# Optimization experiments

Measured on AMD Instinct MI355X. Metric: run time of the kernel, lower is better.

Reference implementation:

```python
import jax, jax.numpy as jnp
import numpy as np

MAX_DEPTH = 12  # 2^12-1 = 4095 internal nodes, 4096 leaves
NUM_INPUT = 1024
NUM_OUTPUT = 1024
BATCH = 4096


def setup_inputs() -> dict:
    key = jax.random.key(0)
    k1, k2, k3 = jax.random.split(key, 3)
    n_internal = (1 << MAX_DEPTH) - 1
    n_leaves = 1 << MAX_DEPTH
    x = jax.random.normal(k1, (BATCH, NUM_INPUT), dtype=jnp.float32)
    # per-node weights ~ N(0, 0.1) as in nn.Parameter(torch.empty(num_input).normal_(0, 0.1))
    W = jax.random.normal(k2, (n_internal, NUM_INPUT), dtype=jnp.float32) * 0.1
    b = jnp.zeros((n_internal,), dtype=jnp.float32)
    # leaf prob_dist initialized to ones in the original
    leaf = jnp.ones((n_leaves, NUM_OUTPUT), dtype=jnp.float32)
    # use random leaves so the blend is non-trivial for correctness checking
    leaf = leaf + jax.random.normal(k3, (n_leaves, NUM_OUTPUT), dtype=jnp.float32)
    return {"x": x, "W": W, "b": b, "leaf": leaf}


def reference(x, W, b, leaf):
    # W rows are internal nodes in level order: [root | level1 (2) | level2 (4) | ...]
    # Gate value at each node: sigmoid(x . w + b); output blends right with weight g,
    # left with weight (1-g), recursively -> leaf mixture weights are products of
    # gate / (1-gate) along each root-to-leaf path.
    B = x.shape[0]
    g = jax.nn.sigmoid(jnp.einsum('bi,ni->bn', x, W) + b)  # [B, n_internal]
    probs = jnp.ones((B, 1), dtype=x.dtype)
    idx = 0
    for d in range(MAX_DEPTH):  # structural loop over tree levels (fixed, small)
        n = 1 << d
        gl = g[:, idx:idx + n]  # gates at level d, [B, n]
        idx += n
        # children interleaved: [L0, R0, L1, R1, ...]; left weight (1-g), right g
        probs = jnp.stack([probs * (1.0 - gl), probs * gl], axis=-1).reshape(B, 2 * n)
    # output = sum over leaves of path_prob * leaf_dist
    out = jnp.einsum('bl,lo->bo', probs, leaf)  # [B, num_output]
    return out
```

## Files before the change

kernel.cpp:

```cpp
#include <hip/hip_runtime.h>
#include <hip/hip_bf16.h>
#include <hip/hip_fp16.h>

typedef _Float16 half8 __attribute__((ext_vector_type(8)));
typedef _Float16 half4 __attribute__((ext_vector_type(4)));
typedef float floatx4 __attribute__((ext_vector_type(4)));

#define BATCH   4096
#define NIN     1024
#define NODES   4095
#define NPAD    4096
#define NOUT    1024
#define NLEAF   4096
#define SPLITK  4

__device__ __forceinline__ void gload_lds16(const void* g, void* l) {
    __builtin_amdgcn_global_load_lds(
        (const __attribute__((address_space(1))) void*)g,
        (__attribute__((address_space(3))) void*)l, 16, 0, 0);
}

__global__ void k_f32_to_f16_pad(const float* __restrict__ src,
                                 _Float16* __restrict__ dst, int n, int nsrc) {
    int i = (blockIdx.x * blockDim.x + threadIdx.x) * 4;
    if (i >= n) return;
    float4 v;
    if (i < nsrc) v = *(const float4*)(src + i);
    else          v = make_float4(0.f, 0.f, 0.f, 0.f);
    half4 h;
    h.x = (_Float16)v.x; h.y = (_Float16)v.y;
    h.z = (_Float16)v.z; h.w = (_Float16)v.w;
    *(half4*)(dst + i) = h;
}

__global__ void k_transpose_f16(const float* __restrict__ src,
                                _Float16* __restrict__ dst) {
    __shared__ _Float16 t[32][33];
    int l0 = blockIdx.x * 32, o0 = blockIdx.y * 32;
    int tx = threadIdx.x & 31, ty = threadIdx.x >> 5;
#pragma unroll
    for (int i = 0; i < 4; i++) {
        int l = l0 + ty + i * 8;
        t[ty + i * 8][tx] = (_Float16)src[(size_t)l * NOUT + o0 + tx];
    }
    __syncthreads();
#pragma unroll
    for (int i = 0; i < 4; i++) {
        int o = o0 + ty + i * 8;
        dst[(size_t)o * NLEAF + l0 + tx] = t[tx][ty + i * 8];
    }
}

template <int EPILOGUE>
__launch_bounds__(1024, 4)
__global__ void gemm256(const _Float16* __restrict__ A,
                        const _Float16* __restrict__ Bm,
                        const float* __restrict__ bias,
                        void* __restrict__ C,
                        int M, int N, int K, int ldc, int Klen) {
    __shared__ __align__(16) _Float16 As[2][2][2][4096];
    __shared__ __align__(16) _Float16 Bs[2][2][2][4096];
    const int tid  = threadIdx.x;
    const int lane = tid & 63;
    const int wid  = tid >> 6;
    const int wm   = wid >> 2;
    const int wn   = wid & 3;
    const int m0 = blockIdx.y * 256;
    const int n0 = blockIdx.x * 256;
    const int k0 = blockIdx.z * Klen;
    (void)N;

    floatx4 acc[4][4] = {};

    const int hh = tid >> 9;
    const int rr = (tid >> 2) & 127;
    const int pp = tid & 3;
    const int cc = pp ^ ((tid >> 3) & 3);
    const _Float16* Abase = A  + (size_t)(m0 + hh * 128 + rr) * K + k0 + cc * 8;
    const _Float16* Bbase = Bm + (size_t)(n0 + hh * 128 + rr) * K + k0 + cc * 8;
    const int dsl = (tid & 511) * 8;

    auto stageA = [&](int bufx, int s, int T) {
        gload_lds16(Abase + T * 64 + s * 32, &As[bufx][hh][s][dsl]);
    };
    auto stageB = [&](int bufx, int s, int T) {
        gload_lds16(Bbase + T * 64 + s * 32, &Bs[bufx][hh][s][dsl]);
    };

    const int l15 = lane & 15;
    const int l4  = lane >> 4;
    const int pos = (l4 ^ ((l15 >> 1) & 3)) * 8;
    const int ra  = (wm & 1) * 64 + l15;
    const int rb  = (wn & 1) * 64 + l15;
    const int ah  = wm >> 1;
    const int bh  = wn >> 1;

    const int NTt = Klen >> 6;

    stageA(0, 0, 0); stageA(0, 1, 0); stageB(0, 0, 0); stageB(0, 1, 0);
    __syncthreads();

    int buf = 0;
    for (int T = 0; T < NTt; ++T) {
        if (T + 1 < NTt) {
            stageA(buf ^ 1, 0, T + 1); stageA(buf ^ 1, 1, T + 1);
            stageB(buf ^ 1, 0, T + 1); stageB(buf ^ 1, 1, T + 1);
        }
#pragma unroll
        for (int s = 0; s < 2; s++) {
            const _Float16* Ab = &As[buf][ah][s][0];
            const _Float16* Bb = &Bs[buf][bh][s][0];
            half8 af[4], bf[4];
#pragma unroll
            for (int fi = 0; fi < 4; fi++)
                af[fi] = *(const half8*)(Ab + (ra + fi * 16) * 32 + pos);
#pragma unroll
            for (int fj = 0; fj < 4; fj++)
                bf[fj] = *(const half8*)(Bb + (rb + fj * 16) * 32 + pos);
#pragma unroll
            for (int fi = 0; fi < 4; fi++)
#pragma unroll
                for (int fj = 0; fj < 4; fj++)
                    acc[fi][fj] = __builtin_amdgcn_mfma_f32_16x16x32_f16(
                        af[fi], bf[fj], acc[fi][fj], 0, 0, 0);
        }
        __syncthreads();
        buf ^= 1;
    }

    _Float16* Cp = (_Float16*)C + (EPILOGUE == 2 ? (size_t)blockIdx.z * M * ldc : 0);
#pragma unroll
    for (int fi = 0; fi < 4; fi++)
#pragma unroll
        for (int fj = 0; fj < 4; fj++) {
            const int col = n0 + wn * 64 + fj * 16 + l15;
            float bb = 0.f;
            if (EPILOGUE == 1) bb = (col < NODES) ? bias[col] : 0.f;
#pragma unroll
            for (int rj = 0; rj < 4; rj++) {
                const int row = m0 + wm * 64 + fi * 16 + l4 * 4 + rj;
                float v = acc[fi][fj][rj];
                if (EPILOGUE == 1) {
                    float z = v + bb;
                    Cp[(size_t)row * ldc + col] = (_Float16)(1.f / (1.f + __expf(-z)));
                } else {
                    Cp[(size_t)row * ldc + col] = (_Float16)v;
                }
            }
        }
}

__global__ void k_reduce4(const _Float16* __restrict__ part, float* __restrict__ out) {
    const size_t S = (size_t)BATCH * NOUT;
    size_t i = ((size_t)blockIdx.x * 256 + threadIdx.x) * 8;
    half8 a = *(const half8*)(part + i);
    half8 b = *(const half8*)(part + S + i);
    half8 c = *(const half8*)(part + 2 * S + i);
    half8 d = *(const half8*)(part + 3 * S + i);
    float4 lo, hi;
    lo.x = (float)a[0] + (float)b[0] + (float)c[0] + (float)d[0];
    lo.y = (float)a[1] + (float)b[1] + (float)c[1] + (float)d[1];
    lo.z = (float)a[2] + (float)b[2] + (float)c[2] + (float)d[2];
    lo.w = (float)a[3] + (float)b[3] + (float)c[3] + (float)d[3];
    hi.x = (float)a[4] + (float)b[4] + (float)c[4] + (float)d[4];
    hi.y = (float)a[5] + (float)b[5] + (float)c[5] + (float)d[5];
    hi.z = (float)a[6] + (float)b[6] + (float)c[6] + (float)d[6];
    hi.w = (float)a[7] + (float)b[7] + (float)c[7] + (float)d[7];
    *(float4*)(out + i) = lo;
    *(float4*)(out + i + 4) = hi;
}

__global__ void k_probs(const _Float16* __restrict__ g,
                        _Float16* __restrict__ probs) {
    __shared__ float gs[NPAD];
    const int b = blockIdx.x;
    const _Float16* grow = g + (size_t)b * NPAD;
#pragma unroll
    for (int it = 0; it < 2; it++) {
        int i = threadIdx.x + it * 256;
        half8 v = *(const half8*)(grow + i * 8);
#pragma unroll
        for (int j = 0; j < 8; j++) gs[i * 8 + j] = (float)v[j];
    }
    __syncthreads();
    const int t = threadIdx.x;
    float p = 1.f;
#pragma unroll
    for (int d = 0; d < 8; d++) {
        int node = (1 << d) - 1 + (t >> (8 - d));
        float gg = gs[node];
        int bit = (t >> (7 - d)) & 1;
        p *= bit ? gg : (1.f - gg);
    }
    float p9[2], p10[4], p11[8], p12[16];
    {
        float gg = gs[255 + t];
        p9[0] = p * (1.f - gg); p9[1] = p * gg;
    }
#pragma unroll
    for (int i = 0; i < 2; i++) {
        float gg = gs[511 + 2 * t + i];
        p10[2 * i] = p9[i] * (1.f - gg); p10[2 * i + 1] = p9[i] * gg;
    }
#pragma unroll
    for (int i = 0; i < 4; i++) {
        float gg = gs[1023 + 4 * t + i];
        p11[2 * i] = p10[i] * (1.f - gg); p11[2 * i + 1] = p10[i] * gg;
    }
#pragma unroll
    for (int i = 0; i < 8; i++) {
        float gg = gs[2047 + 8 * t + i];
        p12[2 * i] = p11[i] * (1.f - gg); p12[2 * i + 1] = p11[i] * gg;
    }
    half8 o0, o1;
#pragma unroll
    for (int j = 0; j < 8; j++) { o0[j] = (_Float16)p12[j]; o1[j] = (_Float16)p12[8 + j]; }
    _Float16* pr = probs + (size_t)b * NLEAF + t * 16;
    *(half8*)(pr) = o0;
    *(half8*)(pr + 8) = o1;
}

extern "C" void kernel_launch(void* const* d_in, const int* in_sizes, int n_in,
                              void* d_out, int out_size, void* d_ws, size_t ws_size,
                              hipStream_t stream) {
    (void)in_sizes; (void)n_in; (void)out_size; (void)ws_size;
    const float* x    = (const float*)d_in[0];
    const float* W    = (const float*)d_in[1];
    const float* bias = (const float*)d_in[2];
    const float* leaf = (const float*)d_in[3];
    float* out = (float*)d_out;

    _Float16* base  = (_Float16*)d_ws;
    _Float16* leafT = base;
    _Float16* probs = base + (size_t)4 * 1024 * 1024;
    _Float16* xh    = base + (size_t)20 * 1024 * 1024;
    _Float16* Wh    = base + (size_t)24 * 1024 * 1024;
    _Float16* g     = base + (size_t)28 * 1024 * 1024;
    _Float16* part  = xh;

    k_f32_to_f16_pad<<<(BATCH * NIN / 4 + 255) / 256, 256, 0, stream>>>(
        x, xh, BATCH * NIN, BATCH * NIN);
    k_f32_to_f16_pad<<<(NPAD * NIN / 4 + 255) / 256, 256, 0, stream>>>(
        W, Wh, NPAD * NIN, NODES * NIN);
    k_transpose_f16<<<dim3(NLEAF / 32, NOUT / 32), 256, 0, stream>>>(leaf, leafT);

    gemm256<1><<<dim3(NPAD / 256, BATCH / 256, 1), 1024, 0, stream>>>(
        xh, Wh, bias, (void*)g, BATCH, NPAD, NIN, NPAD, NIN);

    k_probs<<<BATCH, 256, 0, stream>>>(g, probs);

    gemm256<2><<<dim3(NOUT / 256, BATCH / 256, SPLITK), 1024, 0, stream>>>(
        probs, leafT, nullptr, (void*)part, BATCH, NOUT, NLEAF, NOUT, NLEAF / SPLITK);

    k_reduce4<<<(BATCH * NOUT) / (256 * 8), 256, 0, stream>>>(part, out);
}
```

Baseline: 120.8 us.

## Shrink GEMM tile to 128x256 with 512 threads and K-step of 32

Replaces the 256x256 tile, 1024-thread GEMM with a 128x256 tile run by 512 threads (8 waves). Each main-loop iteration now stages a single 32-wide K slice instead of two, which halves LDS use per block and doubles the number of blocks. The aim is better occupancy and CU coverage: the first GEMM goes from 256 to 512 blocks and the second from 256 to 512 blocks including split-K. In exchange, less data is reused per block, the loop runs twice as many iterations, and there are twice as many barriers per unit of K.

```diff
diff --git a/kernel.cpp b/kernel.cpp
--- a/kernel.cpp
+++ b/kernel.cpp
@@ -52,78 +52,68 @@
 }
 
 template <int EPILOGUE>
-__launch_bounds__(1024, 4)
-__global__ void gemm256(const _Float16* __restrict__ A,
+__launch_bounds__(512, 4)
+__global__ void gemm128(const _Float16* __restrict__ A,
                         const _Float16* __restrict__ Bm,
                         const float* __restrict__ bias,
                         void* __restrict__ C,
                         int M, int N, int K, int ldc, int Klen) {
-    __shared__ __align__(16) _Float16 As[2][2][2][4096];
-    __shared__ __align__(16) _Float16 Bs[2][2][2][4096];
+    __shared__ __align__(16) _Float16 As[2][128 * 32];
+    __shared__ __align__(16) _Float16 Bs[2][256 * 32];
     const int tid  = threadIdx.x;
     const int lane = tid & 63;
     const int wid  = tid >> 6;
     const int wm   = wid >> 2;
     const int wn   = wid & 3;
-    const int m0 = blockIdx.y * 256;
+    const int m0 = blockIdx.y * 128;
     const int n0 = blockIdx.x * 256;
     const int k0 = blockIdx.z * Klen;
     (void)N;
 
     floatx4 acc[4][4] = {};
 
-    const int hh = tid >> 9;
-    const int rr = (tid >> 2) & 127;
+    const int rr = tid >> 2;
     const int pp = tid & 3;
     const int cc = pp ^ ((tid >> 3) & 3);
-    const _Float16* Abase = A  + (size_t)(m0 + hh * 128 + rr) * K + k0 + cc * 8;
-    const _Float16* Bbase = Bm + (size_t)(n0 + hh * 128 + rr) * K + k0 + cc * 8;
-    const int dsl = (tid & 511) * 8;
-
-    auto stageA = [&](int bufx, int s, int T) {
-        gload_lds16(Abase + T * 64 + s * 32, &As[bufx][hh][s][dsl]);
-    };
-    auto stageB = [&](int bufx, int s, int T) {
-        gload_lds16(Bbase + T * 64 + s * 32, &Bs[bufx][hh][s][dsl]);
+    const _Float16* Abase  = A  + (size_t)(m0 + rr) * K + k0 + cc * 8;
+    const _Float16* Bbase  = Bm + (size_t)(n0 + rr) * K + k0 + cc * 8;
+    const _Float16* Bbase2 = Bbase + (size_t)128 * K;
+
+    auto stage = [&](int bufx, int T) {
+        gload_lds16(Abase  + T * 32, &As[bufx][tid * 8]);
+        gload_lds16(Bbase  + T * 32, &Bs[bufx][tid * 8]);
+        gload_lds16(Bbase2 + T * 32, &Bs[bufx][4096 + tid * 8]);
     };
 
     const int l15 = lane & 15;
     const int l4  = lane >> 4;
     const int pos = (l4 ^ ((l15 >> 1) & 3)) * 8;
-    const int ra  = (wm & 1) * 64 + l15;
-    const int rb  = (wn & 1) * 64 + l15;
-    const int ah  = wm >> 1;
-    const int bh  = wn >> 1;
-
-    const int NTt = Klen >> 6;
-
-    stageA(0, 0, 0); stageA(0, 1, 0); stageB(0, 0, 0); stageB(0, 1, 0);
+    const int ra  = wm * 64 + l15;
+    const int rb  = wn * 64 + l15;
+
+    const int NTt = Klen >> 5;
+
+    stage(0, 0);
     __syncthreads();
 
     int buf = 0;
     for (int T = 0; T < NTt; ++T) {
-        if (T + 1 < NTt) {
-            stageA(buf ^ 1, 0, T + 1); stageA(buf ^ 1, 1, T + 1);
-            stageB(buf ^ 1, 0, T + 1); stageB(buf ^ 1, 1, T + 1);
-        }
-#pragma unroll
-        for (int s = 0; s < 2; s++) {
-            const _Float16* Ab = &As[buf][ah][s][0];
-            const _Float16* Bb = &Bs[buf][bh][s][0];
-            half8 af[4], bf[4];
-#pragma unroll
-            for (int fi = 0; fi < 4; fi++)
-                af[fi] = *(const half8*)(Ab + (ra + fi * 16) * 32 + pos);
+        if (T + 1 < NTt) stage(buf ^ 1, T + 1);
+        const _Float16* Ab = &As[buf][0];
+        const _Float16* Bb = &Bs[buf][0];
+        half8 af[4], bf[4];
+#pragma unroll
+        for (int fi = 0; fi < 4; fi++)
+            af[fi] = *(const half8*)(Ab + (ra + fi * 16) * 32 + pos);
+#pragma unroll
+        for (int fj = 0; fj < 4; fj++)
+            bf[fj] = *(const half8*)(Bb + (rb + fj * 16) * 32 + pos);
+#pragma unroll
+        for (int fi = 0; fi < 4; fi++)
 #pragma unroll
             for (int fj = 0; fj < 4; fj++)
-                bf[fj] = *(const half8*)(Bb + (rb + fj * 16) * 32 + pos);
-#pragma unroll
-            for (int fi = 0; fi < 4; fi++)
-#pragma unroll
-                for (int fj = 0; fj < 4; fj++)
-                    acc[fi][fj] = __builtin_amdgcn_mfma_f32_16x16x32_f16(
-                        af[fi], bf[fj], acc[fi][fj], 0, 0, 0);
-        }
+                acc[fi][fj] = __builtin_amdgcn_mfma_f32_16x16x32_f16(
+                    af[fi], bf[fj], acc[fi][fj], 0, 0, 0);
         __syncthreads();
         buf ^= 1;
     }
@@ -244,12 +234,12 @@
         W, Wh, NPAD * NIN, NODES * NIN);
     k_transpose_f16<<<dim3(NLEAF / 32, NOUT / 32), 256, 0, stream>>>(leaf, leafT);
 
-    gemm256<1><<<dim3(NPAD / 256, BATCH / 256, 1), 1024, 0, stream>>>(
+    gemm128<1><<<dim3(NPAD / 256, BATCH / 128, 1), 512, 0, stream>>>(
         xh, Wh, bias, (void*)g, BATCH, NPAD, NIN, NPAD, NIN);
 
     k_probs<<<BATCH, 256, 0, stream>>>(g, probs);
 
-    gemm256<2><<<dim3(NOUT / 256, BATCH / 256, SPLITK), 1024, 0, stream>>>(
+    gemm128<2><<<dim3(NOUT / 256, BATCH / 128, SPLITK), 512, 0, stream>>>(
         probs, leafT, nullptr, (void*)part, BATCH, NOUT, NLEAF, NOUT, NLEAF / SPLITK);
 
     k_reduce4<<<(BATCH * NOUT) / (256 * 8), 256, 0, stream>>>(part, out);
```

Measured after the change: 128.8 us. +6.6%, slower.
